# Performance work log

Hardware: AMD Instinct MI355X
Metric: run time of the kernel (lower is better)

## Reference

```python
import jax, jax.numpy as jnp
import numpy as np

K = 9          # temporal window (kernel_size)
PAD = (K - 1) // 2
BN_EPS = 1e-5


def setup_inputs() -> dict:
    key = jax.random.key(0)
    ks = jax.random.split(key, 9)
    N, Cin, Cout, T, V = 16, 64, 128, 256, 25
    return {
        "x": jax.random.normal(ks[0], (N, Cin, T, V), jnp.float32),
        "conv_w": jax.random.normal(ks[1], (Cout, Cin), jnp.float32) * (1.0 / np.sqrt(Cin)),
        "conv_b": jax.random.normal(ks[2], (Cout,), jnp.float32) * 0.01,
        "gamma": jax.random.uniform(ks[3], (Cout,), jnp.float32, 0.5, 1.5),
        "beta": jax.random.normal(ks[4], (Cout,), jnp.float32) * 0.1,
        "run_mean": jax.random.normal(ks[5], (Cout,), jnp.float32) * 0.1,
        "run_var": jax.random.uniform(ks[6], (Cout,), jnp.float32, 0.5, 1.5),
        "att0": jnp.full((1, Cout, 1, K), 1.0 / K, jnp.float32),
        "A": jax.random.uniform(ks[7], (V, V), jnp.float32),
        "keep_prob": 1,
    }


def reference(x, conv_w, conv_b, gamma, beta, run_mean, run_var, att0, A, keep_prob):
    # 1x1 conv (pointwise channel mix); AvgPool2d((1,1)) is identity for stride=1
    x = jnp.einsum("nctv,oc->notv", x, conv_w) + conv_b[None, :, None, None]
    # BatchNorm2d (eval mode: running stats)
    scale = gamma / jnp.sqrt(run_var + BN_EPS)
    x = x * scale[None, :, None, None] + (beta - run_mean * scale)[None, :, None, None]
    N, C, T, V = x.shape
    # UnfoldTemporalWindows: zero-pad T, gather K temporal shifts -> (N, C, T, K, V)
    xp = jnp.pad(x, ((0, 0), (0, 0), (PAD, PAD), (0, 0)))
    upfold = jnp.stack([xp[:, :, u:u + T, :] for u in range(K)], axis=3)
    # local attention: score each window position against the center frame
    scores = jnp.einsum("nctv,nctuv->nctu", x, upfold) / V
    attn = jax.nn.softmax(scores, axis=-1) + att0
    out = jnp.einsum("nctuv,nctu->nctv", upfold, attn)
    # dropS / dropT are identity at keep_prob == 1 (inference)
    return out
```

## Files before the change

kernel.cpp:

```cpp
#include <hip/hip_runtime.h>
#include <hip/hip_bf16.h>

#define CIN   64
#define COUT  128
#define TT    256
#define VV    25
#define TV    (TT * VV)
#define KW    9
#define PAD   4
#define YROW  32
#define YSTR  (TT * YROW)

typedef __attribute__((ext_vector_type(8))) short short8;
typedef __attribute__((ext_vector_type(4))) float f32x4;

__device__ __forceinline__ unsigned f2b(float f) {
    unsigned u = __builtin_bit_cast(unsigned, f);
    return (u + 0x7FFFu + ((u >> 16) & 1u)) >> 16;
}
__device__ __forceinline__ float lof(unsigned u) {
    return __builtin_bit_cast(float, u << 16);
}
__device__ __forceinline__ float hif(unsigned u) {
    return __builtin_bit_cast(float, u & 0xffff0000u);
}
__device__ __forceinline__ void unpack8(uint4 u, float* d) {
    d[0] = lof(u.x); d[1] = hif(u.x); d[2] = lof(u.y); d[3] = hif(u.y);
    d[4] = lof(u.z); d[5] = hif(u.z); d[6] = lof(u.w); d[7] = hif(u.w);
}
__device__ __forceinline__ int swz(int row, int cbyte) {
    return row * 128 + ((cbyte & ~15) ^ ((row & 7) << 4)) + (cbyte & 15);
}

__global__ __launch_bounds__(256) void conv_mfma(
    const float* __restrict__ x, const float* __restrict__ w,
    const float* __restrict__ cb, const float* __restrict__ gamma,
    const float* __restrict__ beta, const float* __restrict__ rm,
    const float* __restrict__ rv, unsigned short* __restrict__ y)
{
    __shared__ __align__(16) unsigned short Wl[COUT * 64];
    __shared__ __align__(16) unsigned short Xl[128 * 64];
    __shared__ float sc[COUT];
    __shared__ float of[COUT];

    const int pc  = blockIdx.x;
    const int n   = blockIdx.y;
    const int tid = threadIdx.x;
    const int posbase = pc * 128;

    if (tid < COUT) {
        const float s = gamma[tid] * rsqrtf(rv[tid] + 1e-5f);
        sc[tid] = s;
        of[tid] = cb[tid] * s + beta[tid] - rm[tid] * s;
    }
    for (int idx = tid; idx < 2048; idx += 256) {
        const int c4 = idx & 15, o = idx >> 4;
        const f32x4 wv = *(const f32x4*)(w + o * 64 + c4 * 4);
        uint2 pk;
        pk.x = f2b(wv.x) | (f2b(wv.y) << 16);
        pk.y = f2b(wv.z) | (f2b(wv.w) << 16);
        *(uint2*)((char*)Wl + swz(o, c4 * 8)) = pk;
    }
    for (int idx = tid; idx < 2048; idx += 256) {
        const int pos = idx & 127, c4 = idx >> 7;
        const float* xp = x + (size_t)n * CIN * TV + (size_t)(c4 * 4) * TV + posbase + pos;
        const float a0 = xp[0], a1 = xp[TV], a2 = xp[2 * TV], a3 = xp[3 * TV];
        uint2 pk;
        pk.x = f2b(a0) | (f2b(a1) << 16);
        pk.y = f2b(a2) | (f2b(a3) << 16);
        *(uint2*)((char*)Xl + swz(pos, c4 * 8)) = pk;
    }
    __syncthreads();

    const int wv_ = tid >> 6, lane = tid & 63;
    const int lr = lane & 15, lh = lane >> 4;

    short8 afr[2][2];
#pragma unroll
    for (int m0 = 0; m0 < 2; ++m0)
#pragma unroll
        for (int kh = 0; kh < 2; ++kh)
            afr[m0][kh] = *(const short8*)((const char*)Wl +
                              swz(wv_ * 32 + m0 * 16 + lr, kh * 64 + lh * 16));

    f32x4 acc[2][8];
#pragma unroll
    for (int m0 = 0; m0 < 2; ++m0)
#pragma unroll
        for (int n0 = 0; n0 < 8; ++n0) acc[m0][n0] = (f32x4){0.f, 0.f, 0.f, 0.f};

#pragma unroll
    for (int n0 = 0; n0 < 8; ++n0) {
        const int prow = n0 * 16 + lr;
        const short8 b0 = *(const short8*)((const char*)Xl + swz(prow, lh * 16));
        const short8 b1 = *(const short8*)((const char*)Xl + swz(prow, 64 + lh * 16));
#pragma unroll
        for (int m0 = 0; m0 < 2; ++m0) {
            acc[m0][n0] = __builtin_amdgcn_mfma_f32_16x16x32_bf16(afr[m0][0], b0, acc[m0][n0], 0, 0, 0);
            acc[m0][n0] = __builtin_amdgcn_mfma_f32_16x16x32_bf16(afr[m0][1], b1, acc[m0][n0], 0, 0, 0);
        }
    }

    const size_t ybase = (size_t)(n * COUT) * YSTR;
#pragma unroll
    for (int m0 = 0; m0 < 2; ++m0)
#pragma unroll
        for (int n0 = 0; n0 < 8; ++n0)
#pragma unroll
            for (int r = 0; r < 4; ++r) {
                const int o = wv_ * 32 + m0 * 16 + lh * 4 + r;
                const int pos = posbase + n0 * 16 + lr;
                const int t = pos / 25;
                const int v = pos - t * 25;
                const float val = acc[m0][n0][r] * sc[o] + of[o];
                y[ybase + (size_t)o * YSTR + t * YROW + v] = (unsigned short)f2b(val);
            }
}

__global__ __launch_bounds__(128) void attn_kernel(
    const unsigned short* __restrict__ y, const float* __restrict__ att0,
    float* __restrict__ out)
{
    __shared__ __align__(16) float sm[TV];
    __shared__ float a0s[KW];

    uint4* tile = (uint4*)sm;

    const int nc  = blockIdx.x;
    const int c   = nc & (COUT - 1);
    const int tid = threadIdx.x;

    if (tid < KW) a0s[tid] = att0[c * KW + tid];

    if (tid < 32) {
        const int pi = tid >> 3;
        const int p  = (pi < 2) ? pi : (128 + pi);
        tile[p * 8 + (tid & 7)] = make_uint4(0, 0, 0, 0);
    }

    const uint4* yg = (const uint4*)(y + (size_t)nc * YSTR);
#pragma unroll
    for (int i = 0; i < 8; ++i) {
        const int ci = tid + i * 128;
        const int sp = 2 + (ci >> 3);
        const int h8 = (ci & 7) ^ (sp & 7);
        const int r  = ((sp - 2) << 1) | (h8 >> 2);
        const int q  = h8 & 3;
        tile[16 + ci] = yg[r * 4 + q];
    }
    __syncthreads();

    const int t0 = tid * 2;

#define LOADROW(rp, dst)                                                   \
    {                                                                      \
        const int s_ = (rp) >> 1, e_ = s_ & 7, hb_ = ((rp) & 1) << 2;      \
        const uint4 u0 = tile[s_ * 8 + ((hb_ | 0) ^ e_)];                  \
        const uint4 u1 = tile[s_ * 8 + ((hb_ | 1) ^ e_)];                  \
        const uint4 u2 = tile[s_ * 8 + ((hb_ | 2) ^ e_)];                  \
        const uint4 u3 = tile[s_ * 8 + ((hb_ | 3) ^ e_)];                  \
        unpack8(u0, (dst) + 0); unpack8(u1, (dst) + 8);                    \
        unpack8(u2, (dst) + 16); (dst)[24] = lof(u3.x);                    \
    }

    float q0[25], q1[25];
    LOADROW(t0 + 4, q0);
    LOADROW(t0 + 5, q1);

    float s0[KW], s1[KW];
#pragma unroll
    for (int j = 0; j < 10; ++j) {
        const int rp = t0 + j;
        float row[25];
        LOADROW(rp, row);
        float d0 = 0.f, d1 = 0.f;
#pragma unroll
        for (int v = 0; v < 25; ++v) {
            d0 = fmaf(row[v], q0[v], d0);
            d1 = fmaf(row[v], q1[v], d1);
        }
        if (j <= 8) s0[j]     = d0 * (1.0f / 25.0f);
        if (j >= 1) s1[j - 1] = d1 * (1.0f / 25.0f);
    }

    {
        float m0 = s0[0], m1 = s1[0];
#pragma unroll
        for (int u = 1; u < KW; ++u) { m0 = fmaxf(m0, s0[u]); m1 = fmaxf(m1, s1[u]); }
        float d0 = 0.f, d1 = 0.f;
#pragma unroll
        for (int u = 0; u < KW; ++u) {
            s0[u] = __expf(s0[u] - m0); d0 += s0[u];
            s1[u] = __expf(s1[u] - m1); d1 += s1[u];
        }
        const float i0 = 1.f / d0, i1 = 1.f / d1;
#pragma unroll
        for (int u = 0; u < KW; ++u) {
            s0[u] = s0[u] * i0 + a0s[u];
            s1[u] = s1[u] * i1 + a0s[u];
        }
    }

    float o0[25], o1[25];
#pragma unroll
    for (int v = 0; v < 25; ++v) { o0[v] = 0.f; o1[v] = 0.f; }
#pragma unroll
    for (int j = 0; j < 10; ++j) {
        const int rp = t0 + j;
        float row[25];
        LOADROW(rp, row);
        if (j <= 8) {
            const float a = s0[j];
#pragma unroll
            for (int v = 0; v < 25; ++v) o0[v] = fmaf(a, row[v], o0[v]);
        }
        if (j >= 1) {
            const float a = s1[j - 1];
#pragma unroll
            for (int v = 0; v < 25; ++v) o1[v] = fmaf(a, row[v], o1[v]);
        }
    }
#undef LOADROW

    __syncthreads();
    {
        float* dst = &sm[t0 * 25];
#pragma unroll
        for (int k = 0; k < 25; ++k) {
            const int j0 = 2 * k, j1 = 2 * k + 1;
            const float a = (j0 < 25) ? o0[j0] : o1[j0 - 25];
            const float b = (j1 < 25) ? o0[j1] : o1[j1 - 25];
            *(float2*)(dst + j0) = make_float2(a, b);
        }
    }
    __syncthreads();

    {
        float4* og = (float4*)(out + (size_t)nc * TV);
        const float4* sm4 = (const float4*)sm;
        for (int i = tid; i < TV / 4; i += 128) og[i] = sm4[i];
    }
}

extern "C" void kernel_launch(void* const* d_in, const int* in_sizes, int n_in,
                              void* d_out, int out_size, void* d_ws, size_t ws_size,
                              hipStream_t stream)
{
    const float* x     = (const float*)d_in[0];
    const float* w     = (const float*)d_in[1];
    const float* cb    = (const float*)d_in[2];
    const float* gamma = (const float*)d_in[3];
    const float* beta  = (const float*)d_in[4];
    const float* rm    = (const float*)d_in[5];
    const float* rv    = (const float*)d_in[6];
    const float* att0  = (const float*)d_in[7];
    float* out = (float*)d_out;
    unsigned short* y = (unsigned short*)d_ws;

    dim3 gA(TV / 128, 16);
    conv_mfma<<<gA, 256, 0, stream>>>(x, w, cb, gamma, beta, rm, rv, y);

    dim3 gB(16 * COUT);
    attn_kernel<<<gB, 128, 0, stream>>>(y, att0, out);
}
```

Before: 50.02 us.

## Shrink intermediate row stride to 28 and reuse center rows in attention

Cuts the bf16 intermediate row padding from 32 to 28 elements. Each pair of time rows now packs into 7 contiguous uint4s, so the attention kernel loads the tile with plain linear copies instead of a swizzled scatter. The attention kernel reuses the already-loaded center rows for the self and neighbour scores and output terms, skipping two row loads and unpacks per pass. It also splits the dot products into two accumulators for more instruction-level parallelism and hoists the BN scale and offset into registers in the conv epilogue. The unswizzled LDS reads may cause more bank conflicts, and the rows are no longer 16-byte aligned per row.

```diff
diff --git a/kernel.cpp b/kernel.cpp
--- a/kernel.cpp
+++ b/kernel.cpp
@@ -8,7 +8,7 @@
 #define TV    (TT * VV)
 #define KW    9
 #define PAD   4
-#define YROW  32
+#define YROW  28
 #define YSTR  (TT * YROW)
 
 typedef __attribute__((ext_vector_type(8))) short short8;
@@ -23,10 +23,6 @@
 }
 __device__ __forceinline__ float hif(unsigned u) {
     return __builtin_bit_cast(float, u & 0xffff0000u);
-}
-__device__ __forceinline__ void unpack8(uint4 u, float* d) {
-    d[0] = lof(u.x); d[1] = hif(u.x); d[2] = lof(u.y); d[3] = hif(u.y);
-    d[4] = lof(u.z); d[5] = hif(u.z); d[6] = lof(u.w); d[7] = hif(u.w);
 }
 __device__ __forceinline__ int swz(int row, int cbyte) {
     return row * 128 + ((cbyte & ~15) ^ ((row & 7) << 4)) + (cbyte & 15);
@@ -101,6 +97,16 @@
         }
     }
 
+    float scv[2][4], ofv[2][4];
+#pragma unroll
+    for (int m0 = 0; m0 < 2; ++m0)
+#pragma unroll
+        for (int r = 0; r < 4; ++r) {
+            const int o = wv_ * 32 + m0 * 16 + lh * 4 + r;
+            scv[m0][r] = sc[o];
+            ofv[m0][r] = of[o];
+        }
+
     const size_t ybase = (size_t)(n * COUT) * YSTR;
 #pragma unroll
     for (int m0 = 0; m0 < 2; ++m0)
@@ -112,10 +118,25 @@
                 const int pos = posbase + n0 * 16 + lr;
                 const int t = pos / 25;
                 const int v = pos - t * 25;
-                const float val = acc[m0][n0][r] * sc[o] + of[o];
+                const float val = acc[m0][n0][r] * scv[m0][r] + ofv[m0][r];
                 y[ybase + (size_t)o * YSTR + t * YROW + v] = (unsigned short)f2b(val);
             }
 }
+
+#define UC(u,cc) ((cc)==0?(u).x:((cc)==1?(u).y:((cc)==2?(u).z:(u).w)))
+#define DW(k) ((k)<4?UC(u0_,(k)):((k)<8?UC(u1_,(k)-4):((k)<12?UC(u2_,(k)-8):UC(u3_,(k)-12))))
+#define LOADROW(rl, par, dst)                                               \
+    {                                                                       \
+        const int ub_ = (7 * (rl) - (par)) >> 1;                            \
+        const uint4 u0_ = tl[ub_], u1_ = tl[ub_ + 1];                       \
+        const uint4 u2_ = tl[ub_ + 2], u3_ = tl[ub_ + 3];                   \
+        _Pragma("unroll")                                                   \
+        for (int v_ = 0; v_ < 25; ++v_) {                                   \
+            const int k_ = 2 * (par) + (v_ >> 1);                           \
+            const unsigned dw_ = DW(k_);                                    \
+            (dst)[v_] = (v_ & 1) ? hif(dw_) : lof(dw_);                     \
+        }                                                                   \
+    }
 
 __global__ __launch_bounds__(128) void attn_kernel(
     const unsigned short* __restrict__ y, const float* __restrict__ att0,
@@ -124,7 +145,7 @@
     __shared__ __align__(16) float sm[TV];
     __shared__ float a0s[KW];
 
-    uint4* tile = (uint4*)sm;
+    uint4* tl = (uint4*)sm;
 
     const int nc  = blockIdx.x;
     const int c   = nc & (COUT - 1);
@@ -132,55 +153,60 @@
 
     if (tid < KW) a0s[tid] = att0[c * KW + tid];
 
-    if (tid < 32) {
-        const int pi = tid >> 3;
-        const int p  = (pi < 2) ? pi : (128 + pi);
-        tile[p * 8 + (tid & 7)] = make_uint4(0, 0, 0, 0);
-    }
-
+    if (tid < 28) {
+        const int i = (tid < 14) ? tid : (896 + tid);
+        tl[i] = make_uint4(0, 0, 0, 0);
+    }
     const uint4* yg = (const uint4*)(y + (size_t)nc * YSTR);
 #pragma unroll
-    for (int i = 0; i < 8; ++i) {
-        const int ci = tid + i * 128;
-        const int sp = 2 + (ci >> 3);
-        const int h8 = (ci & 7) ^ (sp & 7);
-        const int r  = ((sp - 2) << 1) | (h8 >> 2);
-        const int q  = h8 & 3;
-        tile[16 + ci] = yg[r * 4 + q];
-    }
+    for (int i = 0; i < 7; ++i) tl[14 + tid + i * 128] = yg[tid + i * 128];
     __syncthreads();
 
     const int t0 = tid * 2;
 
-#define LOADROW(rp, dst)                                                   \
-    {                                                                      \
-        const int s_ = (rp) >> 1, e_ = s_ & 7, hb_ = ((rp) & 1) << 2;      \
-        const uint4 u0 = tile[s_ * 8 + ((hb_ | 0) ^ e_)];                  \
-        const uint4 u1 = tile[s_ * 8 + ((hb_ | 1) ^ e_)];                  \
-        const uint4 u2 = tile[s_ * 8 + ((hb_ | 2) ^ e_)];                  \
-        const uint4 u3 = tile[s_ * 8 + ((hb_ | 3) ^ e_)];                  \
-        unpack8(u0, (dst) + 0); unpack8(u1, (dst) + 8);                    \
-        unpack8(u2, (dst) + 16); (dst)[24] = lof(u3.x);                    \
-    }
-
     float q0[25], q1[25];
-    LOADROW(t0 + 4, q0);
-    LOADROW(t0 + 5, q1);
+    LOADROW(t0 + 4, 0, q0);
+    LOADROW(t0 + 5, 1, q1);
 
     float s0[KW], s1[KW];
+    {
+        float a0_ = 0.f, a1_ = 0.f, b0_ = 0.f, b1_ = 0.f, c0_ = 0.f, c1_ = 0.f;
+#pragma unroll
+        for (int v = 0; v < 12; ++v) {
+            a0_ = fmaf(q0[v], q0[v], a0_);
+            b0_ = fmaf(q0[v], q1[v], b0_);
+            c0_ = fmaf(q1[v], q1[v], c0_);
+        }
+#pragma unroll
+        for (int v = 12; v < 25; ++v) {
+            a1_ = fmaf(q0[v], q0[v], a1_);
+            b1_ = fmaf(q0[v], q1[v], b1_);
+            c1_ = fmaf(q1[v], q1[v], c1_);
+        }
+        s0[4] = (a0_ + a1_) * (1.f / 25.f);
+        s0[5] = (b0_ + b1_) * (1.f / 25.f);
+        s1[3] = s0[5];
+        s1[4] = (c0_ + c1_) * (1.f / 25.f);
+    }
+
 #pragma unroll
     for (int j = 0; j < 10; ++j) {
-        const int rp = t0 + j;
+        if (j == 4 || j == 5) continue;
         float row[25];
-        LOADROW(rp, row);
-        float d0 = 0.f, d1 = 0.f;
-#pragma unroll
-        for (int v = 0; v < 25; ++v) {
-            d0 = fmaf(row[v], q0[v], d0);
-            d1 = fmaf(row[v], q1[v], d1);
-        }
-        if (j <= 8) s0[j]     = d0 * (1.0f / 25.0f);
-        if (j >= 1) s1[j - 1] = d1 * (1.0f / 25.0f);
+        LOADROW(t0 + j, (j & 1), row);
+        float d0a = 0.f, d0b = 0.f, d1a = 0.f, d1b = 0.f;
+#pragma unroll
+        for (int v = 0; v < 12; ++v) {
+            d0a = fmaf(row[v], q0[v], d0a);
+            d1a = fmaf(row[v], q1[v], d1a);
+        }
+#pragma unroll
+        for (int v = 12; v < 25; ++v) {
+            d0b = fmaf(row[v], q0[v], d0b);
+            d1b = fmaf(row[v], q1[v], d1b);
+        }
+        if (j <= 8) s0[j]     = (d0a + d0b) * (1.f / 25.f);
+        if (j >= 1) s1[j - 1] = (d1a + d1b) * (1.f / 25.f);
     }
 
     {
@@ -203,12 +229,15 @@
 
     float o0[25], o1[25];
 #pragma unroll
-    for (int v = 0; v < 25; ++v) { o0[v] = 0.f; o1[v] = 0.f; }
+    for (int v = 0; v < 25; ++v) {
+        o0[v] = s0[4] * q0[v] + s0[5] * q1[v];
+        o1[v] = s1[3] * q0[v] + s1[4] * q1[v];
+    }
 #pragma unroll
     for (int j = 0; j < 10; ++j) {
-        const int rp = t0 + j;
+        if (j == 4 || j == 5) continue;
         float row[25];
-        LOADROW(rp, row);
+        LOADROW(t0 + j, (j & 1), row);
         if (j <= 8) {
             const float a = s0[j];
 #pragma unroll
@@ -220,7 +249,6 @@
             for (int v = 0; v < 25; ++v) o1[v] = fmaf(a, row[v], o1[v]);
         }
     }
-#undef LOADROW
 
     __syncthreads();
     {
```

New measurement: 48.08 us. -3.9%, faster.
